# Kernel tuning notes

Hardware: AMD Instinct MI355X
Metric: run time of the kernel (lower is better)

## Reference

```python
import jax, jax.numpy as jnp
import numpy as np

N_NODES = 100000   # multiple of 20 (tile factor)
N_BASE = N_NODES // 20
N_EDGES = 3200000  # avg degree 32


def setup_inputs() -> dict:
    key = jax.random.key(0)
    ks = jax.random.split(key, 12)
    x1 = jax.random.normal(ks[0], (N_NODES, 15), dtype=jnp.float32)
    x2 = jax.random.normal(ks[1], (N_BASE, 4), dtype=jnp.float32)
    edges = jax.random.randint(ks[2], (2, N_EDGES), 0, N_NODES, dtype=jnp.int64)
    # params (PyTorch Linear convention: y = x @ W.T + b)
    W1 = jax.random.normal(ks[3], (15, 15), dtype=jnp.float32) * 0.1
    b1 = jax.random.normal(ks[4], (15,), dtype=jnp.float32) * 0.1
    Wg = jax.random.normal(ks[5], (15, 34), dtype=jnp.float32) * 0.1  # GCNConv weight
    bg = jax.random.normal(ks[6], (15,), dtype=jnp.float32) * 0.1
    W3 = jax.random.normal(ks[7], (1, 34), dtype=jnp.float32) * 0.1
    b3 = jax.random.normal(ks[8], (1,), dtype=jnp.float32) * 0.1
    W4 = jax.random.normal(ks[9], (19, 19), dtype=jnp.float32) * 0.1
    b4 = jax.random.normal(ks[10], (19,), dtype=jnp.float32) * 0.1
    return {"x1": x1, "x2": x2, "edges": edges, "W1": W1, "b1": b1,
            "Wg": Wg, "bg": bg, "W3": W3, "b3": b3, "W4": W4, "b4": b4}


def reference(x1, x2, edges, W1, b1, Wg, bg, W3, b3, W4, b4):
    N = x1.shape[0]
    # b = layer4(cat([x1, tile(x2, (20,1))]))
    x2t = jnp.tile(x2, (20, 1))                       # [N, 4]
    b = jnp.concatenate([x1, x2t], axis=1) @ W4.T + b4  # [N, 19]
    a = jax.nn.relu(x1 @ W1.T + b1)                     # [N, 15]

    # GCN normalization with self-loops (PyG GCNConv defaults)
    row = jnp.concatenate([edges[0], jnp.arange(N, dtype=edges.dtype)])
    col = jnp.concatenate([edges[1], jnp.arange(N, dtype=edges.dtype)])
    deg = jax.ops.segment_sum(jnp.ones_like(col, dtype=x1.dtype), col, num_segments=N)
    dinv = jnp.where(deg > 0, deg ** -0.5, 0.0)
    norm = dinv[row] * dinv[col]                       # [E+N]

    for _ in range(5):
        h = jnp.concatenate([a, b], axis=1) @ Wg.T     # [N, 15]
        agg = jax.ops.segment_sum(h[row] * norm[:, None], col, num_segments=N)
        a = jax.nn.relu(agg + bg)

    out = jnp.concatenate([a, b], axis=1) @ W3.T + b3  # [N, 1]
    return jnp.tanh(out.mean())
```

## Files before the change

kernel.cpp:

```cpp
#include <hip/hip_runtime.h>
#include <hip/hip_fp16.h>
#include <math.h>

#define N_NODES 100000
#define N_BASE  5000
#define N_EDGES 3200000
#define NBKT    391
#define CAPB    9472
#define EPB     4096
#define GEB     782

__device__ inline unsigned pkh(float a, float b) {
    return (unsigned)__half_as_ushort(__float2half_rn(a)) |
           ((unsigned)__half_as_ushort(__float2half_rn(b)) << 16);
}

__device__ inline unsigned hadd2u(unsigned a, unsigned b) {
    __half2 r = __hadd2(*(__half2*)&a, *(__half2*)&b);
    return *(unsigned*)&r;
}

__global__ __launch_bounds__(512) void k_initg(int* __restrict__ gcur, float* __restrict__ bins) {
    int t = threadIdx.x;
    if (t < NBKT) gcur[t] = t * CAPB;
    if (t < 64) bins[t] = 0.0f;
}

__global__ __launch_bounds__(512) void k_bucket(const int* __restrict__ row, const int* __restrict__ col,
                                                int* __restrict__ gcur, unsigned* __restrict__ csr) {
    __shared__ int hist[NBKT], gbase[NBKT], curi[NBKT], excl[NBKT];
    __shared__ int sc[512];
    __shared__ unsigned sdst[EPB];
    __shared__ int sadr[EPB];
    int t = threadIdx.x;
    int e0 = blockIdx.x * EPB;
    int cnt = (N_EDGES - e0 < EPB) ? (N_EDGES - e0) : EPB;
    for (int k = t; k < NBKT; k += 512) hist[k] = 0;
    __syncthreads();
    for (int j = t; j < cnt; j += 512) atomicAdd(&hist[col[e0 + j] >> 8], 1);
    __syncthreads();
    sc[t] = (t < NBKT) ? hist[t] : 0;
    __syncthreads();
    for (int off = 1; off < 512; off <<= 1) {
        int v = (t >= off) ? sc[t - off] : 0;
        __syncthreads();
        sc[t] += v;
        __syncthreads();
    }
    if (t < NBKT) {
        int e = sc[t] - hist[t];
        excl[t] = e;
        curi[t] = e;
        gbase[t] = (hist[t] > 0) ? atomicAdd(&gcur[t], hist[t]) : 0;
    }
    __syncthreads();
    for (int j = t; j < cnt; j += 512) {
        int d = col[e0 + j];
        int s = row[e0 + j];
        int b = d >> 8;
        int pos = atomicAdd(&curi[b], 1);
        sdst[pos] = ((unsigned)(d & 255) << 17) | (unsigned)s;
        sadr[pos] = gbase[b] + (pos - excl[b]);
    }
    __syncthreads();
    for (int j = t; j < cnt; j += 512) csr[sadr[j]] = sdst[j];
}

__global__ __launch_bounds__(1024) void k_sort(const int* __restrict__ gcur, unsigned* __restrict__ csr,
                                               int* __restrict__ rs, int* __restrict__ re,
                                               float* __restrict__ dinv) {
    __shared__ unsigned stage[CAPB];
    __shared__ int hist[256], offs[256], cur[256];
    int t = threadIdx.x, b = blockIdx.x;
    int base = b * CAPB;
    int cnt = gcur[b] - base;
    if (t < 256) hist[t] = 0;
    for (int j = t; j < cnt; j += 1024) stage[j] = csr[base + j];
    __syncthreads();
    for (int j = t; j < cnt; j += 1024) atomicAdd(&hist[stage[j] >> 17], 1);
    __syncthreads();
    if (t < 256) offs[t] = hist[t];
    __syncthreads();
    for (int off = 1; off < 256; off <<= 1) {
        int v = 0;
        if (t < 256 && t >= off) v = offs[t - off];
        __syncthreads();
        if (t < 256) offs[t] += v;
        __syncthreads();
    }
    if (t < 256) {
        int excl = offs[t] - hist[t];
        cur[t] = excl;
        int node = b * 256 + t;
        if (node < N_NODES) {
            rs[node] = base + excl;
            re[node] = base + excl + hist[t];
            dinv[node] = rsqrtf((float)(hist[t] + 1));
        }
    }
    __syncthreads();
    for (int j = t; j < cnt; j += 1024) {
        unsigned p = stage[j];
        int slot = atomicAdd(&cur[p >> 17], 1);
        csr[base + slot] = p & 0x1FFFFu;
    }
}

__global__ __launch_bounds__(256) void k_ab_h(const float* __restrict__ x1, const float* __restrict__ x2,
                                              const float* __restrict__ W1, const float* __restrict__ b1,
                                              const float* __restrict__ W4, const float* __restrict__ b4,
                                              const float* __restrict__ Wg, const float* __restrict__ W3,
                                              const float* __restrict__ dinv,
                                              float* __restrict__ bb, __half* __restrict__ h0,
                                              float* __restrict__ bins) {
    __shared__ float sW1[225], sb1[15], sW4[361], sb4[19], sWg[510], sW3b[19];
    for (int t = threadIdx.x; t < 225; t += 256) sW1[t] = W1[t];
    for (int t = threadIdx.x; t < 361; t += 256) sW4[t] = W4[t];
    for (int t = threadIdx.x; t < 510; t += 256) sWg[t] = Wg[t];
    if (threadIdx.x < 15) sb1[threadIdx.x] = b1[threadIdx.x];
    if (threadIdx.x < 19) { sb4[threadIdx.x] = b4[threadIdx.x]; sW3b[threadIdx.x] = W3[15 + threadIdx.x]; }
    __syncthreads();
    int i = blockIdx.x * 256 + threadIdx.x;
    bool valid = i < N_NODES;
    int ii = valid ? i : 0;
    float x[15];
#pragma unroll
    for (int k = 0; k < 15; k++) x[k] = x1[(size_t)ii * 15 + k];
    float xt[4];
    int ib = ii % N_BASE;
#pragma unroll
    for (int k = 0; k < 4; k++) xt[k] = x2[(size_t)ib * 4 + k];
    float in[34];
    float bp = 0.0f;
#pragma unroll
    for (int o = 0; o < 19; o++) {
        float s = sb4[o];
#pragma unroll
        for (int k = 0; k < 15; k++) s += x[k] * sW4[o * 19 + k];
#pragma unroll
        for (int k = 0; k < 4; k++) s += xt[k] * sW4[o * 19 + 15 + k];
        in[15 + o] = s;
        bp += s * sW3b[o];
    }
#pragma unroll
    for (int o = 0; o < 15; o++) {
        float s = sb1[o];
#pragma unroll
        for (int k = 0; k < 15; k++) s += x[k] * sW1[o * 15 + k];
        in[o] = fmaxf(s, 0.0f);
    }
    float dn = dinv[ii];
    if (valid) {
        float4* bbp = (float4*)(bb + (size_t)ii * 20);
        bbp[0] = make_float4(in[15], in[16], in[17], in[18]);
        bbp[1] = make_float4(in[19], in[20], in[21], in[22]);
        bbp[2] = make_float4(in[23], in[24], in[25], in[26]);
        bbp[3] = make_float4(in[27], in[28], in[29], in[30]);
        bbp[4] = make_float4(in[31], in[32], in[33], 0.0f);
        float hv[15];
#pragma unroll
        for (int o = 0; o < 15; o++) {
            float s = 0.0f;
#pragma unroll
            for (int k = 0; k < 34; k++) s += in[k] * sWg[o * 34 + k];
            hv[o] = s * dn;
        }
        unsigned hu[8];
#pragma unroll
        for (int k = 0; k < 7; k++) hu[k] = pkh(hv[2 * k], hv[2 * k + 1]);
        hu[7] = pkh(hv[14], 0.0f);
        uint4* hp = (uint4*)(h0 + (size_t)ii * 16);
        hp[0] = make_uint4(hu[0], hu[1], hu[2], hu[3]);
        hp[1] = make_uint4(hu[4], hu[5], hu[6], hu[7]);
    }
    float val = valid ? bp : 0.0f;
#pragma unroll
    for (int off = 32; off > 0; off >>= 1) val += __shfl_down(val, off, 64);
    __shared__ float wsum[4];
    if ((threadIdx.x & 63) == 0) wsum[threadIdx.x >> 6] = val;
    __syncthreads();
    if (threadIdx.x == 0) atomicAdd(&bins[blockIdx.x & 63], wsum[0] + wsum[1] + wsum[2] + wsum[3]);
}

__global__ __launch_bounds__(1024) void k_gather(const int* __restrict__ rs, const int* __restrict__ re,
                                                 const unsigned* __restrict__ csr,
                                                 const __half* __restrict__ h_in,
                                                 const float* __restrict__ dinv,
                                                 const float* __restrict__ bb,
                                                 const float* __restrict__ Wg,
                                                 const float* __restrict__ bg,
                                                 const float* __restrict__ W3,
                                                 __half* __restrict__ h_out,
                                                 float* __restrict__ bins, int last) {
    __shared__ float sWg[544], sbg[16], sW3[16];
    __shared__ float sa[16][16];
    __shared__ float ws2[16];
    int t = threadIdx.x;
    for (int k = t; k < 544; k += 1024) sWg[k] = (k < 510) ? Wg[k] : 0.0f;
    if (t < 16) { sbg[t] = (t < 15) ? bg[t] : 0.0f; sW3[t] = (t < 15) ? W3[t] : 0.0f; }
    __syncthreads();
    int wid = t >> 6;
    int node = blockIdx.x * 16 + wid;
    int lane = t & 63, es = lane >> 1, half = lane & 1;
    int start = rs[node];
    int deg = re[node] - start;
    const uint4* hp4 = (const uint4*)h_in;
    uint4 sv = make_uint4(0u, 0u, 0u, 0u);
    if (es == 0) sv = hp4[(size_t)node * 2 + half];
    unsigned a0 = sv.x, a1 = sv.y, a2 = sv.z, a3 = sv.w;
    for (int base = 0; base < deg; base += 64) {
        int rem = deg - base;
        int lim = rem < 64 ? rem : 64;
        unsigned ce = 0;
        if (lane < lim) ce = csr[start + base + lane];
        unsigned pa = __shfl(ce, es, 64);
        uint4 va = make_uint4(0u, 0u, 0u, 0u);
        if (es < lim) va = hp4[(size_t)pa * 2 + half];
        if (lim > 32) {
            unsigned pb = __shfl(ce, es + 32, 64);
            uint4 vb = make_uint4(0u, 0u, 0u, 0u);
            if (es + 32 < lim) vb = hp4[(size_t)pb * 2 + half];
            a0 = hadd2u(a0, va.x); a1 = hadd2u(a1, va.y);
            a2 = hadd2u(a2, va.z); a3 = hadd2u(a3, va.w);
            a0 = hadd2u(a0, vb.x); a1 = hadd2u(a1, vb.y);
            a2 = hadd2u(a2, vb.z); a3 = hadd2u(a3, vb.w);
        } else {
            a0 = hadd2u(a0, va.x); a1 = hadd2u(a1, va.y);
            a2 = hadd2u(a2, va.z); a3 = hadd2u(a3, va.w);
        }
    }
    int sel2 = (lane >> 1) & 1;
    unsigned s0 = sel2 ? a0 : a2;
    unsigned s1 = sel2 ? a1 : a3;
    unsigned k0 = sel2 ? a2 : a0;
    unsigned k1 = sel2 ? a3 : a1;
    k0 = hadd2u(k0, __shfl_xor(s0, 2, 64));
    k1 = hadd2u(k1, __shfl_xor(s1, 2, 64));
    int sel4 = (lane >> 2) & 1;
    unsigned sd = sel4 ? k0 : k1;
    unsigned kk = sel4 ? k1 : k0;
    kk = hadd2u(kk, __shfl_xor(sd, 4, 64));
    kk = hadd2u(kk, __shfl_xor(kk, 8, 64));
    kk = hadd2u(kk, __shfl_xor(kk, 16, 64));
    kk = hadd2u(kk, __shfl_xor(kk, 32, 64));
    int pr = 4 * half + 2 * sel2 + sel4;
    float2 fsum = __half22float2(*(__half2*)&kk);
    float dn = dinv[node];
    float avx = fmaxf(dn * fsum.x + sbg[2 * pr], 0.0f);
    float avy = fmaxf(dn * fsum.y + sbg[2 * pr + 1], 0.0f);
    if (lane < 8) { sa[wid][2 * pr] = avx; sa[wid][2 * pr + 1] = avy; }
    __syncthreads();
    if (!last) {
        int c2e = lane & 7, p = lane >> 3;
        int o0 = 2 * c2e;
        float inv0 = sa[wid][p];
        float inv1 = (p < 7) ? sa[wid][p + 8] : bb[(size_t)node * 20 + 0];
        float s0e = inv0 * sWg[o0 * 34 + p]       + inv1 * sWg[o0 * 34 + p + 8];
        float s1e = inv0 * sWg[(o0 + 1) * 34 + p] + inv1 * sWg[(o0 + 1) * 34 + p + 8];
#pragma unroll
        for (int i = 2; i < 5; i++) {
            int k = p + 8 * i;
            if (k < 34) {
                float inv = bb[(size_t)node * 20 + (k - 15)];
                s0e += inv * sWg[o0 * 34 + k];
                s1e += inv * sWg[(o0 + 1) * 34 + k];
            }
        }
        s0e += __shfl_xor(s0e, 8, 64);
        s1e += __shfl_xor(s1e, 8, 64);
        s0e += __shfl_xor(s0e, 16, 64);
        s1e += __shfl_xor(s1e, 16, 64);
        s0e += __shfl_xor(s0e, 32, 64);
        s1e += __shfl_xor(s1e, 32, 64);
        if (p == 0)
            ((unsigned*)h_out)[(size_t)node * 8 + c2e] = pkh(s0e * dn, s1e * dn);
    } else {
        float c = 0.0f;
        if (lane < 8) c = avx * sW3[2 * pr] + avy * sW3[2 * pr + 1];
        c += __shfl_xor(c, 1, 64);
        c += __shfl_xor(c, 2, 64);
        c += __shfl_xor(c, 4, 64);
        if (lane == 0) ws2[wid] = c;
        __syncthreads();
        if (t == 0) {
            float s = 0.0f;
#pragma unroll
            for (int k = 0; k < 16; k++) s += ws2[k];
            atomicAdd(&bins[blockIdx.x & 63], s);
        }
    }
}

__global__ void k_finalize(const float* __restrict__ bins, const float* __restrict__ b3,
                           float* __restrict__ out) {
    float s = 0.0f;
    for (int k = 0; k < 64; k++) s += bins[k];
    out[0] = tanhf(s * (1.0f / (float)N_NODES) + b3[0]);
}

extern "C" void kernel_launch(void* const* d_in, const int* in_sizes, int n_in,
                              void* d_out, int out_size, void* d_ws, size_t ws_size,
                              hipStream_t stream) {
    const float* x1 = (const float*)d_in[0];
    const float* x2 = (const float*)d_in[1];
    const int* edges = (const int*)d_in[2];
    const float* W1 = (const float*)d_in[3];
    const float* b1 = (const float*)d_in[4];
    const float* Wg = (const float*)d_in[5];
    const float* bg = (const float*)d_in[6];
    const float* W3 = (const float*)d_in[7];
    const float* b3 = (const float*)d_in[8];
    const float* W4 = (const float*)d_in[9];
    const float* b4 = (const float*)d_in[10];

    const int* row = edges;
    const int* col = edges + N_EDGES;

    char* ws = (char*)d_ws;
    unsigned* csr  = (unsigned*)ws;
    float*    bb   = (float*)(csr + (size_t)NBKT * CAPB);
    __half*   h0   = (__half*)(bb + (size_t)N_NODES * 20);
    __half*   h1   = h0 + (size_t)N_NODES * 16;
    float*    dinv = (float*)(h1 + (size_t)N_NODES * 16);
    int*      rs   = (int*)(dinv + N_NODES);
    int*      re   = rs + N_NODES;
    int*      gcur = re + N_NODES;
    float*    bins = (float*)(gcur + NBKT);

    int gN = (N_NODES + 255) / 256;

    k_initg<<<1, 512, 0, stream>>>(gcur, bins);
    k_bucket<<<GEB, 512, 0, stream>>>(row, col, gcur, csr);
    k_sort<<<NBKT, 1024, 0, stream>>>(gcur, csr, rs, re, dinv);
    k_ab_h<<<gN, 256, 0, stream>>>(x1, x2, W1, b1, W4, b4, Wg, W3, dinv, bb, h0, bins);
    for (int t = 0; t < 5; t++) {
        const __half* hi = (t & 1) ? h1 : h0;
        __half* ho = (t & 1) ? h0 : h1;
        k_gather<<<N_NODES / 16, 1024, 0, stream>>>(rs, re, csr, hi, dinv, bb, Wg, bg, W3,
                                                    ho, bins, t == 4 ? 1 : 0);
    }
    k_finalize<<<1, 1, 0, stream>>>(bins, b3, (float*)d_out);
}
```

Before: 400.4 us.

## Process two nodes per wavefront in GCN gather and drop shared-memory sync

Each 64-lane wavefront now aggregates two destination nodes at once, with lanes 0-31 loading edge indices for one node and lanes 32-63 for the other, so a degree-32 node no longer leaves half the wave idle. The per-node activation exchange moves from shared memory plus a block barrier to lane shuffles. The grid is halved to match. This costs extra registers and shuffle instructions, and the loop runs to the larger of the two degrees.

```diff
diff --git a/kernel.cpp b/kernel.cpp
--- a/kernel.cpp
+++ b/kernel.cpp
@@ -193,90 +193,126 @@
                                                  __half* __restrict__ h_out,
                                                  float* __restrict__ bins, int last) {
     __shared__ float sWg[544], sbg[16], sW3[16];
-    __shared__ float sa[16][16];
     __shared__ float ws2[16];
     int t = threadIdx.x;
     for (int k = t; k < 544; k += 1024) sWg[k] = (k < 510) ? Wg[k] : 0.0f;
     if (t < 16) { sbg[t] = (t < 15) ? bg[t] : 0.0f; sW3[t] = (t < 15) ? W3[t] : 0.0f; }
     __syncthreads();
     int wid = t >> 6;
-    int node = blockIdx.x * 16 + wid;
+    int n0 = blockIdx.x * 32 + wid * 2;
+    int n1 = n0 + 1;
     int lane = t & 63, es = lane >> 1, half = lane & 1;
-    int start = rs[node];
-    int deg = re[node] - start;
+    int rs0 = rs[n0], deg0 = re[n0] - rs0;
+    int rs1 = rs[n1], deg1 = re[n1] - rs1;
     const uint4* hp4 = (const uint4*)h_in;
-    uint4 sv = make_uint4(0u, 0u, 0u, 0u);
-    if (es == 0) sv = hp4[(size_t)node * 2 + half];
-    unsigned a0 = sv.x, a1 = sv.y, a2 = sv.z, a3 = sv.w;
-    for (int base = 0; base < deg; base += 64) {
-        int rem = deg - base;
-        int lim = rem < 64 ? rem : 64;
+    uint4 s0v = make_uint4(0u, 0u, 0u, 0u), s1v = make_uint4(0u, 0u, 0u, 0u);
+    if (es == 0) s0v = hp4[(size_t)n0 * 2 + half];
+    if (es == 1) s1v = hp4[(size_t)n1 * 2 + half];
+    unsigned a00 = s0v.x, a01 = s0v.y, a02 = s0v.z, a03 = s0v.w;
+    unsigned a10 = s1v.x, a11 = s1v.y, a12 = s1v.z, a13 = s1v.w;
+    int degm = deg0 > deg1 ? deg0 : deg1;
+    for (int base = 0; base < degm; base += 32) {
+        int le = lane & 31;
+        bool hi = lane >= 32;
+        int src = hi ? rs1 : rs0;
+        int dg = hi ? deg1 : deg0;
         unsigned ce = 0;
-        if (lane < lim) ce = csr[start + base + lane];
+        if (base + le < dg) ce = csr[src + base + le];
+        int lim0 = deg0 - base;
+        int lim1 = deg1 - base;
         unsigned pa = __shfl(ce, es, 64);
+        unsigned pb = __shfl(ce, 32 + es, 64);
         uint4 va = make_uint4(0u, 0u, 0u, 0u);
-        if (es < lim) va = hp4[(size_t)pa * 2 + half];
-        if (lim > 32) {
-            unsigned pb = __shfl(ce, es + 32, 64);
-            uint4 vb = make_uint4(0u, 0u, 0u, 0u);
-            if (es + 32 < lim) vb = hp4[(size_t)pb * 2 + half];
-            a0 = hadd2u(a0, va.x); a1 = hadd2u(a1, va.y);
-            a2 = hadd2u(a2, va.z); a3 = hadd2u(a3, va.w);
-            a0 = hadd2u(a0, vb.x); a1 = hadd2u(a1, vb.y);
-            a2 = hadd2u(a2, vb.z); a3 = hadd2u(a3, vb.w);
-        } else {
-            a0 = hadd2u(a0, va.x); a1 = hadd2u(a1, va.y);
-            a2 = hadd2u(a2, va.z); a3 = hadd2u(a3, va.w);
-        }
+        uint4 vb = make_uint4(0u, 0u, 0u, 0u);
+        if (es < lim0) va = hp4[(size_t)pa * 2 + half];
+        if (es < lim1) vb = hp4[(size_t)pb * 2 + half];
+        a00 = hadd2u(a00, va.x); a01 = hadd2u(a01, va.y);
+        a02 = hadd2u(a02, va.z); a03 = hadd2u(a03, va.w);
+        a10 = hadd2u(a10, vb.x); a11 = hadd2u(a11, vb.y);
+        a12 = hadd2u(a12, vb.z); a13 = hadd2u(a13, vb.w);
     }
     int sel2 = (lane >> 1) & 1;
-    unsigned s0 = sel2 ? a0 : a2;
-    unsigned s1 = sel2 ? a1 : a3;
-    unsigned k0 = sel2 ? a2 : a0;
-    unsigned k1 = sel2 ? a3 : a1;
-    k0 = hadd2u(k0, __shfl_xor(s0, 2, 64));
-    k1 = hadd2u(k1, __shfl_xor(s1, 2, 64));
     int sel4 = (lane >> 2) & 1;
-    unsigned sd = sel4 ? k0 : k1;
-    unsigned kk = sel4 ? k1 : k0;
-    kk = hadd2u(kk, __shfl_xor(sd, 4, 64));
-    kk = hadd2u(kk, __shfl_xor(kk, 8, 64));
-    kk = hadd2u(kk, __shfl_xor(kk, 16, 64));
-    kk = hadd2u(kk, __shfl_xor(kk, 32, 64));
+    unsigned kk0, kk1;
+    {
+        unsigned sA = sel2 ? a00 : a02, sB = sel2 ? a01 : a03;
+        unsigned kA = sel2 ? a02 : a00, kB = sel2 ? a03 : a01;
+        kA = hadd2u(kA, __shfl_xor(sA, 2, 64));
+        kB = hadd2u(kB, __shfl_xor(sB, 2, 64));
+        unsigned sd = sel4 ? kA : kB, kc = sel4 ? kB : kA;
+        kc = hadd2u(kc, __shfl_xor(sd, 4, 64));
+        kc = hadd2u(kc, __shfl_xor(kc, 8, 64));
+        kc = hadd2u(kc, __shfl_xor(kc, 16, 64));
+        kc = hadd2u(kc, __shfl_xor(kc, 32, 64));
+        kk0 = kc;
+    }
+    {
+        unsigned sA = sel2 ? a10 : a12, sB = sel2 ? a11 : a13;
+        unsigned kA = sel2 ? a12 : a10, kB = sel2 ? a13 : a11;
+        kA = hadd2u(kA, __shfl_xor(sA, 2, 64));
+        kB = hadd2u(kB, __shfl_xor(sB, 2, 64));
+        unsigned sd = sel4 ? kA : kB, kc = sel4 ? kB : kA;
+        kc = hadd2u(kc, __shfl_xor(sd, 4, 64));
+        kc = hadd2u(kc, __shfl_xor(kc, 8, 64));
+        kc = hadd2u(kc, __shfl_xor(kc, 16, 64));
+        kc = hadd2u(kc, __shfl_xor(kc, 32, 64));
+        kk1 = kc;
+    }
     int pr = 4 * half + 2 * sel2 + sel4;
-    float2 fsum = __half22float2(*(__half2*)&kk);
-    float dn = dinv[node];
-    float avx = fmaxf(dn * fsum.x + sbg[2 * pr], 0.0f);
-    float avy = fmaxf(dn * fsum.y + sbg[2 * pr + 1], 0.0f);
-    if (lane < 8) { sa[wid][2 * pr] = avx; sa[wid][2 * pr + 1] = avy; }
-    __syncthreads();
+    float dn0 = dinv[n0], dn1 = dinv[n1];
+    float2 f0 = __half22float2(*(__half2*)&kk0);
+    float2 f1 = __half22float2(*(__half2*)&kk1);
+    float avx0 = fmaxf(dn0 * f0.x + sbg[2 * pr], 0.0f);
+    float avy0 = fmaxf(dn0 * f0.y + sbg[2 * pr + 1], 0.0f);
+    float avx1 = fmaxf(dn1 * f1.x + sbg[2 * pr], 0.0f);
+    float avy1 = fmaxf(dn1 * f1.y + sbg[2 * pr + 1], 0.0f);
     if (!last) {
-        int c2e = lane & 7, p = lane >> 3;
-        int o0 = 2 * c2e;
-        float inv0 = sa[wid][p];
-        float inv1 = (p < 7) ? sa[wid][p + 8] : bb[(size_t)node * 20 + 0];
-        float s0e = inv0 * sWg[o0 * 34 + p]       + inv1 * sWg[o0 * 34 + p + 8];
-        float s1e = inv0 * sWg[(o0 + 1) * 34 + p] + inv1 * sWg[(o0 + 1) * 34 + p + 8];
+        int p = lane >> 3, c2e = lane & 7, o0 = 2 * c2e;
+        int j0 = p >> 1, j1 = (p + 8) >> 1;
+        int l0 = ((j0 & 1) << 2) | (j0 & 2) | ((j0 >> 2) & 1);
+        int l1 = ((j1 & 1) << 2) | (j1 & 2) | ((j1 >> 2) & 1);
+        float ex0a = __shfl(avx0, l0, 64), ey0a = __shfl(avy0, l0, 64);
+        float ex1a = __shfl(avx0, l1, 64), ey1a = __shfl(avy0, l1, 64);
+        float ex0b = __shfl(avx1, l0, 64), ey0b = __shfl(avy1, l0, 64);
+        float ex1b = __shfl(avx1, l1, 64), ey1b = __shfl(avy1, l1, 64);
+        float inv0a = (p & 1) ? ey0a : ex0a;
+        float inv1a = (p & 1) ? ey1a : ex1a;
+        float inv0b = (p & 1) ? ey0b : ex0b;
+        float inv1b = (p & 1) ? ey1b : ex1b;
+        if (p == 7) { inv1a = bb[(size_t)n0 * 20 + 0]; inv1b = bb[(size_t)n1 * 20 + 0]; }
+        float wq0 = sWg[o0 * 34 + p],       wq1 = sWg[o0 * 34 + p + 8];
+        float wr0 = sWg[(o0 + 1) * 34 + p], wr1 = sWg[(o0 + 1) * 34 + p + 8];
+        float s0a = inv0a * wq0 + inv1a * wq1;
+        float s1a = inv0a * wr0 + inv1a * wr1;
+        float s0b = inv0b * wq0 + inv1b * wq1;
+        float s1b = inv0b * wr0 + inv1b * wr1;
 #pragma unroll
         for (int i = 2; i < 5; i++) {
             int k = p + 8 * i;
             if (k < 34) {
-                float inv = bb[(size_t)node * 20 + (k - 15)];
-                s0e += inv * sWg[o0 * 34 + k];
-                s1e += inv * sWg[(o0 + 1) * 34 + k];
+                float ia = bb[(size_t)n0 * 20 + (k - 15)];
+                float ib2 = bb[(size_t)n1 * 20 + (k - 15)];
+                float w0 = sWg[o0 * 34 + k], w1 = sWg[(o0 + 1) * 34 + k];
+                s0a += ia * w0; s1a += ia * w1;
+                s0b += ib2 * w0; s1b += ib2 * w1;
             }
         }
-        s0e += __shfl_xor(s0e, 8, 64);
-        s1e += __shfl_xor(s1e, 8, 64);
-        s0e += __shfl_xor(s0e, 16, 64);
-        s1e += __shfl_xor(s1e, 16, 64);
-        s0e += __shfl_xor(s0e, 32, 64);
-        s1e += __shfl_xor(s1e, 32, 64);
-        if (p == 0)
-            ((unsigned*)h_out)[(size_t)node * 8 + c2e] = pkh(s0e * dn, s1e * dn);
+        s0a += __shfl_xor(s0a, 8, 64);  s1a += __shfl_xor(s1a, 8, 64);
+        s0a += __shfl_xor(s0a, 16, 64); s1a += __shfl_xor(s1a, 16, 64);
+        s0a += __shfl_xor(s0a, 32, 64); s1a += __shfl_xor(s1a, 32, 64);
+        s0b += __shfl_xor(s0b, 8, 64);  s1b += __shfl_xor(s1b, 8, 64);
+        s0b += __shfl_xor(s0b, 16, 64); s1b += __shfl_xor(s1b, 16, 64);
+        s0b += __shfl_xor(s0b, 32, 64); s1b += __shfl_xor(s1b, 32, 64);
+        if (p == 0) {
+            ((unsigned*)h_out)[(size_t)n0 * 8 + c2e] = pkh(s0a * dn0, s1a * dn0);
+            ((unsigned*)h_out)[(size_t)n1 * 8 + c2e] = pkh(s0b * dn1, s1b * dn1);
+        }
     } else {
         float c = 0.0f;
-        if (lane < 8) c = avx * sW3[2 * pr] + avy * sW3[2 * pr + 1];
+        if (lane < 8) {
+            c = avx0 * sW3[2 * pr] + avy0 * sW3[2 * pr + 1]
+              + avx1 * sW3[2 * pr] + avy1 * sW3[2 * pr + 1];
+        }
         c += __shfl_xor(c, 1, 64);
         c += __shfl_xor(c, 2, 64);
         c += __shfl_xor(c, 4, 64);
@@ -336,7 +372,7 @@
     for (int t = 0; t < 5; t++) {
         const __half* hi = (t & 1) ? h1 : h0;
         __half* ho = (t & 1) ? h0 : h1;
-        k_gather<<<N_NODES / 16, 1024, 0, stream>>>(rs, re, csr, hi, dinv, bb, Wg, bg, W3,
+        k_gather<<<N_NODES / 32, 1024, 0, stream>>>(rs, re, csr, hi, dinv, bb, Wg, bg, W3,
                                                     ho, bins, t == 4 ? 1 : 0);
     }
     k_finalize<<<1, 1, 0, stream>>>(bins, b3, (float*)d_out);
```

Measured after the change: 351.6 us. 1.14x faster.
